# Kernel tuning notes

Measured on AMD Instinct MI355X. Metric: run time of the kernel, lower is better.

The kernel has to match this reference:

```python
import jax, jax.numpy as jnp
import numpy as np

N_LAYERS = 2
N_QUBITS = 4
BATCH = 1048576


def _apply1(state, U, w):
    # state: [B,2,2,2,2]; U: [2,2] (shared) or [B,2,2] (per-sample)
    s = jnp.moveaxis(state, w + 1, -1)
    if U.ndim == 3:
        s = jnp.einsum('bij,b...j->b...i', U, s)
    else:
        s = jnp.einsum('ij,...j->...i', U, s)
    return jnp.moveaxis(s, -1, w + 1)


_CNOT = np.array([[1, 0, 0, 0], [0, 1, 0, 0], [0, 0, 0, 1], [0, 0, 1, 0]], dtype=np.complex64)


def _cnot(state, c, t):
    s = jnp.moveaxis(state, (c + 1, t + 1), (-2, -1))
    sh = s.shape
    s = s.reshape(sh[:-2] + (4,))
    s = jnp.einsum('ij,...j->...i', jnp.asarray(_CNOT), s).reshape(sh)
    return jnp.moveaxis(s, (-2, -1), (c + 1, t + 1))


def _rx(theta):  # theta: [B] -> [B,2,2]
    c = jnp.cos(theta / 2).astype(jnp.complex64)
    s = (-1j * jnp.sin(theta / 2)).astype(jnp.complex64)
    return jnp.stack([jnp.stack([c, s], -1), jnp.stack([s, c], -1)], -2)


def _ry(theta):  # scalar -> [2,2]
    c = jnp.cos(theta / 2).astype(jnp.complex64)
    s = jnp.sin(theta / 2).astype(jnp.complex64)
    return jnp.stack([jnp.stack([c, -s]), jnp.stack([s, c])])


def _rz(theta):  # scalar -> [2,2] diagonal
    em = jnp.exp(-0.5j * theta.astype(jnp.complex64))
    ep = jnp.exp(0.5j * theta.astype(jnp.complex64))
    z = jnp.zeros((), jnp.complex64)
    return jnp.stack([jnp.stack([em, z]), jnp.stack([z, ep])])


def setup_inputs() -> dict:
    key = jax.random.key(0)
    k1, k2 = jax.random.split(key)
    x = jax.random.uniform(k1, (BATCH, N_QUBITS), jnp.float32) * (2.0 * np.pi)
    weights = jax.random.uniform(k2, (N_LAYERS, N_QUBITS, 2), jnp.float32) * (2.0 * np.pi)
    return {"x": x, "weights": weights}


def reference(x, weights):
    B = x.shape[0]
    # |0000> state, batched: [B,2,2,2,2]
    state = jnp.zeros((B, 16), jnp.complex64).at[:, 0].set(1.0)
    state = state.reshape((B,) + (2,) * N_QUBITS)
    for l in range(N_LAYERS):
        for i in range(N_QUBITS):
            state = _apply1(state, _rx(x[:, i]), i)
        for i in range(N_QUBITS):
            state = _apply1(state, _ry(weights[l, i, 0]), i)
            state = _apply1(state, _rz(weights[l, i, 1]), i)
        for i in range(N_QUBITS - 1):
            state = _cnot(state, i, i + 1)
    probs = state.real ** 2 + state.imag ** 2  # [B,2,2,2,2]
    outs = []
    for i in range(N_QUBITS):
        axes = tuple(a for a in range(1, N_QUBITS + 1) if a != i + 1)
        m = probs.sum(axes)  # [B,2]
        outs.append(m[:, 0] - m[:, 1])  # <Z_i>
    return jnp.stack(outs, -1)  # [B,4]
```

## Files before the change

kernel.cpp:

```cpp
#include <hip/hip_runtime.h>


struct C2 { float r, i; };

__device__ __forceinline__ C2 cmul(C2 a, C2 b) {
    C2 o;
    o.r = a.r * b.r - a.i * b.i;
    o.i = a.r * b.i + a.i * b.r;
    return o;
}

__global__ void precompute_gates(const float* __restrict__ w, float* __restrict__ g) {
    int t = threadIdx.x;
    if (t >= 8) return;
    int l = t >> 2, q = t & 3;
    float thy = w[l * 8 + q * 2 + 0];
    float thz = w[l * 8 + q * 2 + 1];
    float cy = cosf(0.5f * thy), sy = sinf(0.5f * thy);
    float cz = cosf(0.5f * thz), sz = sinf(0.5f * thz);
    float* o = g + l * 32 + q * 8;
    if (l == 0) {
        o[0] = cz * cy;  o[1] = -sz * cy;
        o[2] = sz * sy;  o[3] =  cz * sy;
        o[4] = cz * sy;  o[5] =  sz * sy;
        o[6] = sz * cy;  o[7] = -cz * cy;
    } else {
        o[0] =  cz * cy;  o[1] = -sz * cy;
        o[2] = -cz * sy;  o[3] =  sz * sy;
        o[4] =  cz * sy;  o[5] =  sz * sy;
        o[6] =  cz * cy;  o[7] =  sz * cy;
    }
}

__device__ __forceinline__ void cnot_chain(C2 st[16]) {
    #pragma unroll
    for (int j = 0; j < 4; j++) { C2 t = st[8 + j]; st[8 + j] = st[12 + j]; st[12 + j] = t; }
    {
        C2 t;
        t = st[4];  st[4]  = st[6];  st[6]  = t;
        t = st[5];  st[5]  = st[7];  st[7]  = t;
        t = st[12]; st[12] = st[14]; st[14] = t;
        t = st[13]; st[13] = st[15]; st[15] = t;
    }
    {
        C2 t;
        t = st[2];  st[2]  = st[3];  st[3]  = t;
        t = st[6];  st[6]  = st[7];  st[7]  = t;
        t = st[10]; st[10] = st[11]; st[11] = t;
        t = st[14]; st[14] = st[15]; st[15] = t;
    }
}

__global__ void __launch_bounds__(256) qml_kernel(
        const float* __restrict__ x, const float* __restrict__ g,
        float* __restrict__ out, int batch) {
    int tid = blockIdx.x * blockDim.x + threadIdx.x;
    if (tid >= batch) return;

    float4 xv = reinterpret_cast<const float4*>(x)[tid];
    float c[4], s[4];
    __sincosf(0.5f * xv.x, &s[0], &c[0]);
    __sincosf(0.5f * xv.y, &s[1], &c[1]);
    __sincosf(0.5f * xv.z, &s[2], &c[2]);
    __sincosf(0.5f * xv.w, &s[3], &c[3]);

    C2 v[4][2];
    #pragma unroll
    for (int q = 0; q < 4; q++) {
        const float* o = g + q * 8;
        v[q][0].r = c[q] * o[0] + s[q] * o[2];
        v[q][0].i = c[q] * o[1] + s[q] * o[3];
        v[q][1].r = c[q] * o[4] + s[q] * o[6];
        v[q][1].i = c[q] * o[5] + s[q] * o[7];
    }

    C2 t01[4], t23[4], st[16];
    #pragma unroll
    for (int a = 0; a < 2; a++)
        #pragma unroll
        for (int b = 0; b < 2; b++) {
            t01[a * 2 + b] = cmul(v[0][a], v[1][b]);
            t23[a * 2 + b] = cmul(v[2][a], v[3][b]);
        }
    #pragma unroll
    for (int a = 0; a < 4; a++)
        #pragma unroll
        for (int b = 0; b < 4; b++)
            st[a * 4 + b] = cmul(t01[a], t23[b]);

    cnot_chain(st);

    #pragma unroll
    for (int q = 0; q < 4; q++) {
        const float* o = g + 32 + q * 8;
        C2 u00, u01, u10, u11;
        u00.r = c[q] * o[0] + s[q] * o[3];
        u00.i = c[q] * o[1] - s[q] * o[2];
        u01.r = c[q] * o[2] + s[q] * o[1];
        u01.i = c[q] * o[3] - s[q] * o[0];
        u10.r = c[q] * o[4] + s[q] * o[7];
        u10.i = c[q] * o[5] - s[q] * o[6];
        u11.r = c[q] * o[6] + s[q] * o[5];
        u11.i = c[q] * o[7] - s[q] * o[4];
        int bit = 8 >> q;
        #pragma unroll
        for (int n0 = 0; n0 < 16; n0++) {
            if (n0 & bit) continue;
            int n1 = n0 | bit;
            C2 a0 = st[n0], a1 = st[n1];
            st[n0].r = u00.r * a0.r - u00.i * a0.i + u01.r * a1.r - u01.i * a1.i;
            st[n0].i = u00.r * a0.i + u00.i * a0.r + u01.r * a1.i + u01.i * a1.r;
            st[n1].r = u10.r * a0.r - u10.i * a0.i + u11.r * a1.r - u11.i * a1.i;
            st[n1].i = u10.r * a0.i + u10.i * a0.r + u11.r * a1.i + u11.i * a1.r;
        }
    }

    cnot_chain(st);

    float p[16];
    #pragma unroll
    for (int n = 0; n < 16; n++) p[n] = st[n].r * st[n].r + st[n].i * st[n].i;

    float a8[8], z3 = 0.f;
    #pragma unroll
    for (int m = 0; m < 8; m++) { a8[m] = p[2 * m] + p[2 * m + 1]; z3 += p[2 * m] - p[2 * m + 1]; }
    float b4[4], z2 = 0.f;
    #pragma unroll
    for (int k = 0; k < 4; k++) { b4[k] = a8[2 * k] + a8[2 * k + 1]; z2 += a8[2 * k] - a8[2 * k + 1]; }
    float z1 = (b4[0] - b4[1]) + (b4[2] - b4[3]);
    float z0 = (b4[0] + b4[1]) - (b4[2] + b4[3]);

    float4 ov = make_float4(z0, z1, z2, z3);
    reinterpret_cast<float4*>(out)[tid] = ov;
}

extern "C" void kernel_launch(void* const* d_in, const int* in_sizes, int n_in,
                              void* d_out, int out_size, void* d_ws, size_t ws_size,
                              hipStream_t stream) {
    const float* x = (const float*)d_in[0];
    const float* w = (const float*)d_in[1];
    float* out = (float*)d_out;
    float* g = (float*)d_ws;
    int batch = in_sizes[0] / 4;

    precompute_gates<<<1, 64, 0, stream>>>(w, g);
    int block = 256;
    int grid = (batch + block - 1) / block;
    qml_kernel<<<grid, block, 0, stream>>>(x, g, out, batch);
}
```

Baseline: 85.99 us.

## Process two samples per thread, simplify layer-2 gate algebra, use hardware sin/cos

Each thread now handles two batch samples, and the gate table is hoisted into registers once per thread. The second-layer gate (RZ·RY·RX) is reduced algebraically: the RZ phase is dropped because it does not affect Z-basis probabilities, so only cos/sin of the RY angle are stored. The per-sample sin/cos now use the raw AMDGCN sin/cos builtins on x/(4π), which removes the range-reduction code. The aim is to cut ALU work and global-load overhead per sample, at the cost of higher register pressure, half as many threads, and possible precision loss from the hardware transcendentals on larger arguments.

Result: slower. 92.54 us (+7.6%).

```diff
diff --git a/kernel.cpp b/kernel.cpp
--- a/kernel.cpp
+++ b/kernel.cpp
@@ -10,25 +10,26 @@
     return o;
 }
 
+#define INV_4PI 0.07957747154594767f
+
 __global__ void precompute_gates(const float* __restrict__ w, float* __restrict__ g) {
     int t = threadIdx.x;
     if (t >= 8) return;
     int l = t >> 2, q = t & 3;
-    float thy = w[l * 8 + q * 2 + 0];
-    float thz = w[l * 8 + q * 2 + 1];
-    float cy = cosf(0.5f * thy), sy = sinf(0.5f * thy);
-    float cz = cosf(0.5f * thz), sz = sinf(0.5f * thz);
-    float* o = g + l * 32 + q * 8;
     if (l == 0) {
+        float thy = w[q * 2 + 0];
+        float thz = w[q * 2 + 1];
+        float cy = cosf(0.5f * thy), sy = sinf(0.5f * thy);
+        float cz = cosf(0.5f * thz), sz = sinf(0.5f * thz);
+        float* o = g + q * 8;
         o[0] = cz * cy;  o[1] = -sz * cy;
         o[2] = sz * sy;  o[3] =  cz * sy;
         o[4] = cz * sy;  o[5] =  sz * sy;
         o[6] = sz * cy;  o[7] = -cz * cy;
     } else {
-        o[0] =  cz * cy;  o[1] = -sz * cy;
-        o[2] = -cz * sy;  o[3] =  sz * sy;
-        o[4] =  cz * sy;  o[5] =  sz * sy;
-        o[6] =  cz * cy;  o[7] =  sz * cy;
+        float thy = w[8 + q * 2 + 0];
+        g[32 + q * 2 + 0] = cosf(0.5f * thy);
+        g[32 + q * 2 + 1] = sinf(0.5f * thy);
     }
 }
 
@@ -54,84 +55,111 @@
 __global__ void __launch_bounds__(256) qml_kernel(
         const float* __restrict__ x, const float* __restrict__ g,
         float* __restrict__ out, int batch) {
-    int tid = blockIdx.x * blockDim.x + threadIdx.x;
-    if (tid >= batch) return;
+    int base = (blockIdx.x * blockDim.x + threadIdx.x) * 2;
+    if (base >= batch) return;
+    int idx1 = (base + 1 < batch) ? base + 1 : base;
 
-    float4 xv = reinterpret_cast<const float4*>(x)[tid];
-    float c[4], s[4];
-    __sincosf(0.5f * xv.x, &s[0], &c[0]);
-    __sincosf(0.5f * xv.y, &s[1], &c[1]);
-    __sincosf(0.5f * xv.z, &s[2], &c[2]);
-    __sincosf(0.5f * xv.w, &s[3], &c[3]);
+    float l1[32];
+    #pragma unroll
+    for (int j = 0; j < 32; j++) l1[j] = g[j];
+    float cb[4], sb[4];
+    #pragma unroll
+    for (int q = 0; q < 4; q++) { cb[q] = g[32 + q * 2]; sb[q] = g[33 + q * 2]; }
 
-    C2 v[4][2];
+    float4 xv[2];
+    xv[0] = reinterpret_cast<const float4*>(x)[base];
+    xv[1] = reinterpret_cast<const float4*>(x)[idx1];
+
+    float c[2][4], s[2][4];
     #pragma unroll
-    for (int q = 0; q < 4; q++) {
-        const float* o = g + q * 8;
-        v[q][0].r = c[q] * o[0] + s[q] * o[2];
-        v[q][0].i = c[q] * o[1] + s[q] * o[3];
-        v[q][1].r = c[q] * o[4] + s[q] * o[6];
-        v[q][1].i = c[q] * o[5] + s[q] * o[7];
+    for (int k = 0; k < 2; k++) {
+        float xs0 = xv[k].x, xs1 = xv[k].y, xs2 = xv[k].z, xs3 = xv[k].w;
+        float r0 = xs0 * INV_4PI, r1 = xs1 * INV_4PI, r2 = xs2 * INV_4PI, r3 = xs3 * INV_4PI;
+        s[k][0] = __builtin_amdgcn_sinf(r0); c[k][0] = __builtin_amdgcn_cosf(r0);
+        s[k][1] = __builtin_amdgcn_sinf(r1); c[k][1] = __builtin_amdgcn_cosf(r1);
+        s[k][2] = __builtin_amdgcn_sinf(r2); c[k][2] = __builtin_amdgcn_cosf(r2);
+        s[k][3] = __builtin_amdgcn_sinf(r3); c[k][3] = __builtin_amdgcn_cosf(r3);
     }
 
-    C2 t01[4], t23[4], st[16];
+    C2 v[2][4][2];
     #pragma unroll
-    for (int a = 0; a < 2; a++)
+    for (int k = 0; k < 2; k++)
         #pragma unroll
-        for (int b = 0; b < 2; b++) {
-            t01[a * 2 + b] = cmul(v[0][a], v[1][b]);
-            t23[a * 2 + b] = cmul(v[2][a], v[3][b]);
+        for (int q = 0; q < 4; q++) {
+            const float* o = l1 + q * 8;
+            v[k][q][0].r = c[k][q] * o[0] + s[k][q] * o[2];
+            v[k][q][0].i = c[k][q] * o[1] + s[k][q] * o[3];
+            v[k][q][1].r = c[k][q] * o[4] + s[k][q] * o[6];
+            v[k][q][1].i = c[k][q] * o[5] + s[k][q] * o[7];
         }
+
+    C2 st[2][16];
     #pragma unroll
-    for (int a = 0; a < 4; a++)
+    for (int k = 0; k < 2; k++) {
+        C2 t01[4], t23[4];
         #pragma unroll
-        for (int b = 0; b < 4; b++)
-            st[a * 4 + b] = cmul(t01[a], t23[b]);
+        for (int a = 0; a < 2; a++)
+            #pragma unroll
+            for (int b = 0; b < 2; b++) {
+                t01[a * 2 + b] = cmul(v[k][0][a], v[k][1][b]);
+                t23[a * 2 + b] = cmul(v[k][2][a], v[k][3][b]);
+            }
+        #pragma unroll
+        for (int a = 0; a < 4; a++)
+            #pragma unroll
+            for (int b = 0; b < 4; b++)
+                st[k][a * 4 + b] = cmul(t01[a], t23[b]);
+    }
 
-    cnot_chain(st);
+    #pragma unroll
+    for (int k = 0; k < 2; k++) cnot_chain(st[k]);
 
     #pragma unroll
     for (int q = 0; q < 4; q++) {
-        const float* o = g + 32 + q * 8;
-        C2 u00, u01, u10, u11;
-        u00.r = c[q] * o[0] + s[q] * o[3];
-        u00.i = c[q] * o[1] - s[q] * o[2];
-        u01.r = c[q] * o[2] + s[q] * o[1];
-        u01.i = c[q] * o[3] - s[q] * o[0];
-        u10.r = c[q] * o[4] + s[q] * o[7];
-        u10.i = c[q] * o[5] - s[q] * o[6];
-        u11.r = c[q] * o[6] + s[q] * o[5];
-        u11.i = c[q] * o[7] - s[q] * o[4];
         int bit = 8 >> q;
         #pragma unroll
-        for (int n0 = 0; n0 < 16; n0++) {
-            if (n0 & bit) continue;
-            int n1 = n0 | bit;
-            C2 a0 = st[n0], a1 = st[n1];
-            st[n0].r = u00.r * a0.r - u00.i * a0.i + u01.r * a1.r - u01.i * a1.i;
-            st[n0].i = u00.r * a0.i + u00.i * a0.r + u01.r * a1.i + u01.i * a1.r;
-            st[n1].r = u10.r * a0.r - u10.i * a0.i + u11.r * a1.r - u11.i * a1.i;
-            st[n1].i = u10.r * a0.i + u10.i * a0.r + u11.r * a1.i + u11.i * a1.r;
+        for (int k = 0; k < 2; k++) {
+            float ar =  cb[q] * c[k][q];
+            float ai =  sb[q] * s[k][q];
+            float br = -sb[q] * c[k][q];
+            float bi = -cb[q] * s[k][q];
+            #pragma unroll
+            for (int n0 = 0; n0 < 16; n0++) {
+                if (n0 & bit) continue;
+                int n1 = n0 | bit;
+                C2 a0 = st[k][n0], a1 = st[k][n1];
+                st[k][n0].r =  ar * a0.r - ai * a0.i + br * a1.r - bi * a1.i;
+                st[k][n0].i =  ar * a0.i + ai * a0.r + br * a1.i + bi * a1.r;
+                st[k][n1].r = -br * a0.r - bi * a0.i + ar * a1.r + ai * a1.i;
+                st[k][n1].i = -br * a0.i + bi * a0.r + ar * a1.i - ai * a1.r;
+            }
         }
     }
 
-    cnot_chain(st);
+    #pragma unroll
+    for (int k = 0; k < 2; k++) cnot_chain(st[k]);
 
-    float p[16];
+    float4 ov[2];
     #pragma unroll
-    for (int n = 0; n < 16; n++) p[n] = st[n].r * st[n].r + st[n].i * st[n].i;
+    for (int k = 0; k < 2; k++) {
+        float p[16];
+        #pragma unroll
+        for (int n = 0; n < 16; n++)
+            p[n] = st[k][n].r * st[k][n].r + st[k][n].i * st[k][n].i;
 
-    float a8[8], z3 = 0.f;
-    #pragma unroll
-    for (int m = 0; m < 8; m++) { a8[m] = p[2 * m] + p[2 * m + 1]; z3 += p[2 * m] - p[2 * m + 1]; }
-    float b4[4], z2 = 0.f;
-    #pragma unroll
-    for (int k = 0; k < 4; k++) { b4[k] = a8[2 * k] + a8[2 * k + 1]; z2 += a8[2 * k] - a8[2 * k + 1]; }
-    float z1 = (b4[0] - b4[1]) + (b4[2] - b4[3]);
-    float z0 = (b4[0] + b4[1]) - (b4[2] + b4[3]);
+        float a8[8], z3 = 0.f;
+        #pragma unroll
+        for (int m = 0; m < 8; m++) { a8[m] = p[2 * m] + p[2 * m + 1]; z3 += p[2 * m] - p[2 * m + 1]; }
+        float b4[4], z2 = 0.f;
+        #pragma unroll
+        for (int kk = 0; kk < 4; kk++) { b4[kk] = a8[2 * kk] + a8[2 * kk + 1]; z2 += a8[2 * kk] - a8[2 * kk + 1]; }
+        float z1 = (b4[0] - b4[1]) + (b4[2] - b4[3]);
+        float z0 = (b4[0] + b4[1]) - (b4[2] + b4[3]);
+        ov[k] = make_float4(z0, z1, z2, z3);
+    }
 
-    float4 ov = make_float4(z0, z1, z2, z3);
-    reinterpret_cast<float4*>(out)[tid] = ov;
+    reinterpret_cast<float4*>(out)[base] = ov[0];
+    reinterpret_cast<float4*>(out)[idx1] = ov[1];
 }
 
 extern "C" void kernel_launch(void* const* d_in, const int* in_sizes, int n_in,
@@ -145,6 +173,7 @@
 
     precompute_gates<<<1, 64, 0, stream>>>(w, g);
     int block = 256;
-    int grid = (batch + block - 1) / block;
+    int threads_needed = (batch + 1) / 2;
+    int grid = (threads_needed + block - 1) / block;
     qml_kernel<<<grid, block, 0, stream>>>(x, g, out, batch);
 }
```

## Eliminate layer-2 RZ phases and final qubit gate algebraically in readout

Applied to the files above, without the earlier changes.

Layer-2 RZ rotations are dropped for qubits 0-2 because diagonal phases before the final CNOTs and Z measurement do not change the expectation values. The last qubit's RX·RY·RZ gate is folded into closed-form coefficients applied to pairwise densities, and the second CNOT chain is absorbed into the reduction signs. Sines and cosines now use the raw hardware sin/cos builtins with a revolution-scaled argument instead of __sincosf. This cuts ALU work per sample in what is likely a memory-bound kernel, at the cost of a derivation that is hard to verify and depends on the hardware trig accuracy.

Result: slower. 94.20 us (+9.5%).

```diff
diff --git a/kernel.cpp b/kernel.cpp
--- a/kernel.cpp
+++ b/kernel.cpp
@@ -10,25 +10,31 @@
     return o;
 }
 
+#define INV_4PI 0.07957747154594767f
+
 __global__ void precompute_gates(const float* __restrict__ w, float* __restrict__ g) {
     int t = threadIdx.x;
     if (t >= 8) return;
     int l = t >> 2, q = t & 3;
-    float thy = w[l * 8 + q * 2 + 0];
-    float thz = w[l * 8 + q * 2 + 1];
-    float cy = cosf(0.5f * thy), sy = sinf(0.5f * thy);
-    float cz = cosf(0.5f * thz), sz = sinf(0.5f * thz);
-    float* o = g + l * 32 + q * 8;
     if (l == 0) {
+        float thy = w[q * 2 + 0];
+        float thz = w[q * 2 + 1];
+        float cy = cosf(0.5f * thy), sy = sinf(0.5f * thy);
+        float cz = cosf(0.5f * thz), sz = sinf(0.5f * thz);
+        float* o = g + q * 8;
         o[0] = cz * cy;  o[1] = -sz * cy;
         o[2] = sz * sy;  o[3] =  cz * sy;
         o[4] = cz * sy;  o[5] =  sz * sy;
         o[6] = sz * cy;  o[7] = -cz * cy;
+    } else if (q < 3) {
+        float thy = w[8 + q * 2 + 0];
+        g[32 + q * 2 + 0] = cosf(0.5f * thy);
+        g[32 + q * 2 + 1] = sinf(0.5f * thy);
     } else {
-        o[0] =  cz * cy;  o[1] = -sz * cy;
-        o[2] = -cz * sy;  o[3] =  sz * sy;
-        o[4] =  cz * sy;  o[5] =  sz * sy;
-        o[6] =  cz * cy;  o[7] =  sz * cy;
+        float thy = w[8 + 3 * 2 + 0];
+        g[40] =  cosf(thy);
+        g[41] = -2.0f * sinf(thy);
+        g[42] =  4.0f * cosf(thy);
     }
 }
 
@@ -59,10 +65,14 @@
 
     float4 xv = reinterpret_cast<const float4*>(x)[tid];
     float c[4], s[4];
-    __sincosf(0.5f * xv.x, &s[0], &c[0]);
-    __sincosf(0.5f * xv.y, &s[1], &c[1]);
-    __sincosf(0.5f * xv.z, &s[2], &c[2]);
-    __sincosf(0.5f * xv.w, &s[3], &c[3]);
+    {
+        float r0 = xv.x * INV_4PI, r1 = xv.y * INV_4PI;
+        float r2 = xv.z * INV_4PI, r3 = xv.w * INV_4PI;
+        s[0] = __builtin_amdgcn_sinf(r0); c[0] = __builtin_amdgcn_cosf(r0);
+        s[1] = __builtin_amdgcn_sinf(r1); c[1] = __builtin_amdgcn_cosf(r1);
+        s[2] = __builtin_amdgcn_sinf(r2); c[2] = __builtin_amdgcn_cosf(r2);
+        s[3] = __builtin_amdgcn_sinf(r3); c[3] = __builtin_amdgcn_cosf(r3);
+    }
 
     C2 v[4][2];
     #pragma unroll
@@ -91,47 +101,59 @@
     cnot_chain(st);
 
     #pragma unroll
-    for (int q = 0; q < 4; q++) {
-        const float* o = g + 32 + q * 8;
-        C2 u00, u01, u10, u11;
-        u00.r = c[q] * o[0] + s[q] * o[3];
-        u00.i = c[q] * o[1] - s[q] * o[2];
-        u01.r = c[q] * o[2] + s[q] * o[1];
-        u01.i = c[q] * o[3] - s[q] * o[0];
-        u10.r = c[q] * o[4] + s[q] * o[7];
-        u10.i = c[q] * o[5] - s[q] * o[6];
-        u11.r = c[q] * o[6] + s[q] * o[5];
-        u11.i = c[q] * o[7] - s[q] * o[4];
+    for (int q = 0; q < 3; q++) {
+        float cb = g[32 + q * 2 + 0];
+        float sb = g[32 + q * 2 + 1];
+        float ar =  cb * c[q];
+        float ai =  sb * s[q];
+        float br = -sb * c[q];
+        float bi = -cb * s[q];
         int bit = 8 >> q;
         #pragma unroll
         for (int n0 = 0; n0 < 16; n0++) {
             if (n0 & bit) continue;
             int n1 = n0 | bit;
             C2 a0 = st[n0], a1 = st[n1];
-            st[n0].r = u00.r * a0.r - u00.i * a0.i + u01.r * a1.r - u01.i * a1.i;
-            st[n0].i = u00.r * a0.i + u00.i * a0.r + u01.r * a1.i + u01.i * a1.r;
-            st[n1].r = u10.r * a0.r - u10.i * a0.i + u11.r * a1.r - u11.i * a1.i;
-            st[n1].i = u10.r * a0.i + u10.i * a0.r + u11.r * a1.i + u11.i * a1.r;
+            st[n0].r =  ar * a0.r - ai * a0.i + br * a1.r - bi * a1.i;
+            st[n0].i =  ar * a0.i + ai * a0.r + br * a1.i + bi * a1.r;
+            st[n1].r = -br * a0.r - bi * a0.i + ar * a1.r + ai * a1.i;
+            st[n1].i = -br * a0.i + bi * a0.r + ar * a1.i - ai * a1.r;
         }
     }
 
-    cnot_chain(st);
+    float m_coef, cu, cv;
+    {
+        float cs2 = __builtin_fmaf(-s[3], s[3], c[3] * c[3]);
+        m_coef = g[40] * cs2;
+        cu = g[41];
+        cv = g[42] * (c[3] * s[3]);
+    }
 
-    float p[16];
+    float S[8], D[8];
     #pragma unroll
-    for (int n = 0; n < 16; n++) p[n] = st[n].r * st[n].r + st[n].i * st[n].i;
+    for (int m = 0; m < 8; m++) {
+        C2 a0 = st[2 * m], a1 = st[2 * m + 1];
+        float q0 = __builtin_fmaf(a0.i, a0.i, a0.r * a0.r);
+        float q1 = __builtin_fmaf(a1.i, a1.i, a1.r * a1.r);
+        float Rc = __builtin_fmaf(a0.i, a1.i, a0.r * a1.r);
+        float Ic = __builtin_fmaf(-a0.i, a1.r, a0.r * a1.i);
+        S[m] = q0 + q1;
+        float dd = q0 - q1;
+        float Dm = m_coef * dd;
+        Dm = __builtin_fmaf(cu, Rc, Dm);
+        Dm = __builtin_fmaf(cv, Ic, Dm);
+        D[m] = Dm;
+    }
 
-    float a8[8], z3 = 0.f;
-    #pragma unroll
-    for (int m = 0; m < 8; m++) { a8[m] = p[2 * m] + p[2 * m + 1]; z3 += p[2 * m] - p[2 * m + 1]; }
-    float b4[4], z2 = 0.f;
-    #pragma unroll
-    for (int k = 0; k < 4; k++) { b4[k] = a8[2 * k] + a8[2 * k + 1]; z2 += a8[2 * k] - a8[2 * k + 1]; }
-    float z1 = (b4[0] - b4[1]) + (b4[2] - b4[3]);
-    float z0 = (b4[0] + b4[1]) - (b4[2] + b4[3]);
+    float e0 = S[0] + S[1], e1 = S[2] + S[3], e2 = S[4] + S[5], e3 = S[6] + S[7];
+    float z0 = (e0 + e1) - (e2 + e3);
+    float z1 = (e0 - e1) - (e2 - e3);
+    float f0 = S[0] - S[1], f1 = S[2] - S[3], f2 = S[4] - S[5], f3 = S[6] - S[7];
+    float z2 = (f0 - f1) - (f2 - f3);
+    float g0 = D[0] - D[1], g1 = D[2] - D[3], g2 = D[4] - D[5], g3 = D[6] - D[7];
+    float z3 = (g0 - g1) - (g2 - g3);
 
-    float4 ov = make_float4(z0, z1, z2, z3);
-    reinterpret_cast<float4*>(out)[tid] = ov;
+    reinterpret_cast<float4*>(out)[tid] = make_float4(z0, z1, z2, z3);
 }
 
 extern "C" void kernel_launch(void* const* d_in, const int* in_sizes, int n_in,
```

## Use packed float2 math and simplify layer-2 gate to RY·RX product form

Applied to the files above, without the earlier changes.

Represents complex amplitudes as 2-wide float vectors so multiplies map to packed FMA instructions (v_pk_fma_f32 on CDNA). The second layer's RZ is dropped from the per-sample gate because diagonal phases before measurement do not affect probabilities. The combined RY·RX matrix is expressed with four real coefficients instead of eight precomputed values. This reduces per-thread ALU work and constant loads, at the risk of extra shuffle/negate instructions if the compiler does not fuse swizzles into packed ops. The kernel is likely memory-bound, so the gain may be small.

Result: slower. 88.25 us (+2.6%).

```diff
diff --git a/kernel.cpp b/kernel.cpp
--- a/kernel.cpp
+++ b/kernel.cpp
@@ -1,49 +1,54 @@
 #include <hip/hip_runtime.h>
 
 
-struct C2 { float r, i; };
+typedef float v2f __attribute__((ext_vector_type(2)));
 
-__device__ __forceinline__ C2 cmul(C2 a, C2 b) {
-    C2 o;
-    o.r = a.r * b.r - a.i * b.i;
-    o.i = a.r * b.i + a.i * b.r;
-    return o;
+__device__ __forceinline__ v2f splat2(float a) { v2f r; r.x = a; r.y = a; return r; }
+
+__device__ __forceinline__ v2f pfma(float a, v2f b, v2f c) {
+    return __builtin_elementwise_fma(splat2(a), b, c);
+}
+
+__device__ __forceinline__ v2f swneg(v2f a) { return __builtin_shufflevector(a, -a, 3, 0); }
+__device__ __forceinline__ v2f swconj(v2f a) { return __builtin_shufflevector(a, -a, 1, 2); }
+
+__device__ __forceinline__ v2f cmul(v2f a, v2f b) {
+    return pfma(a.x, b, splat2(a.y) * swneg(b));
 }
 
 __global__ void precompute_gates(const float* __restrict__ w, float* __restrict__ g) {
     int t = threadIdx.x;
     if (t >= 8) return;
     int l = t >> 2, q = t & 3;
-    float thy = w[l * 8 + q * 2 + 0];
-    float thz = w[l * 8 + q * 2 + 1];
-    float cy = cosf(0.5f * thy), sy = sinf(0.5f * thy);
-    float cz = cosf(0.5f * thz), sz = sinf(0.5f * thz);
-    float* o = g + l * 32 + q * 8;
     if (l == 0) {
+        float thy = w[q * 2 + 0];
+        float thz = w[q * 2 + 1];
+        float cy = cosf(0.5f * thy), sy = sinf(0.5f * thy);
+        float cz = cosf(0.5f * thz), sz = sinf(0.5f * thz);
+        float* o = g + q * 8;
         o[0] = cz * cy;  o[1] = -sz * cy;
         o[2] = sz * sy;  o[3] =  cz * sy;
         o[4] = cz * sy;  o[5] =  sz * sy;
         o[6] = sz * cy;  o[7] = -cz * cy;
     } else {
-        o[0] =  cz * cy;  o[1] = -sz * cy;
-        o[2] = -cz * sy;  o[3] =  sz * sy;
-        o[4] =  cz * sy;  o[5] =  sz * sy;
-        o[6] =  cz * cy;  o[7] =  sz * cy;
+        float thy = w[8 + q * 2 + 0];
+        g[32 + q * 2 + 0] = cosf(0.5f * thy);
+        g[32 + q * 2 + 1] = sinf(0.5f * thy);
     }
 }
 
-__device__ __forceinline__ void cnot_chain(C2 st[16]) {
+__device__ __forceinline__ void cnot_chain(v2f st[16]) {
     #pragma unroll
-    for (int j = 0; j < 4; j++) { C2 t = st[8 + j]; st[8 + j] = st[12 + j]; st[12 + j] = t; }
+    for (int j = 0; j < 4; j++) { v2f t = st[8 + j]; st[8 + j] = st[12 + j]; st[12 + j] = t; }
     {
-        C2 t;
+        v2f t;
         t = st[4];  st[4]  = st[6];  st[6]  = t;
         t = st[5];  st[5]  = st[7];  st[7]  = t;
         t = st[12]; st[12] = st[14]; st[14] = t;
         t = st[13]; st[13] = st[15]; st[15] = t;
     }
     {
-        C2 t;
+        v2f t;
         t = st[2];  st[2]  = st[3];  st[3]  = t;
         t = st[6];  st[6]  = st[7];  st[7]  = t;
         t = st[10]; st[10] = st[11]; st[11] = t;
@@ -64,17 +69,15 @@
     __sincosf(0.5f * xv.z, &s[2], &c[2]);
     __sincosf(0.5f * xv.w, &s[3], &c[3]);
 
-    C2 v[4][2];
+    const v2f* __restrict__ gv = reinterpret_cast<const v2f*>(g);
+    v2f v[4][2];
     #pragma unroll
     for (int q = 0; q < 4; q++) {
-        const float* o = g + q * 8;
-        v[q][0].r = c[q] * o[0] + s[q] * o[2];
-        v[q][0].i = c[q] * o[1] + s[q] * o[3];
-        v[q][1].r = c[q] * o[4] + s[q] * o[6];
-        v[q][1].i = c[q] * o[5] + s[q] * o[7];
+        v[q][0] = pfma(c[q], gv[q * 4 + 0], splat2(s[q]) * gv[q * 4 + 1]);
+        v[q][1] = pfma(c[q], gv[q * 4 + 2], splat2(s[q]) * gv[q * 4 + 3]);
     }
 
-    C2 t01[4], t23[4], st[16];
+    v2f t01[4], t23[4], st[16];
     #pragma unroll
     for (int a = 0; a < 2; a++)
         #pragma unroll
@@ -92,26 +95,23 @@
 
     #pragma unroll
     for (int q = 0; q < 4; q++) {
-        const float* o = g + 32 + q * 8;
-        C2 u00, u01, u10, u11;
-        u00.r = c[q] * o[0] + s[q] * o[3];
-        u00.i = c[q] * o[1] - s[q] * o[2];
-        u01.r = c[q] * o[2] + s[q] * o[1];
-        u01.i = c[q] * o[3] - s[q] * o[0];
-        u10.r = c[q] * o[4] + s[q] * o[7];
-        u10.i = c[q] * o[5] - s[q] * o[6];
-        u11.r = c[q] * o[6] + s[q] * o[5];
-        u11.i = c[q] * o[7] - s[q] * o[4];
+        float cb = g[32 + q * 2 + 0];
+        float sb = g[32 + q * 2 + 1];
+        float ar  = cb * c[q];
+        float ai  = sb * s[q];
+        float nbr = sb * c[q];
+        float nbi = cb * s[q];
+        float br = -nbr, bi = -nbi;
         int bit = 8 >> q;
         #pragma unroll
         for (int n0 = 0; n0 < 16; n0++) {
             if (n0 & bit) continue;
             int n1 = n0 | bit;
-            C2 a0 = st[n0], a1 = st[n1];
-            st[n0].r = u00.r * a0.r - u00.i * a0.i + u01.r * a1.r - u01.i * a1.i;
-            st[n0].i = u00.r * a0.i + u00.i * a0.r + u01.r * a1.i + u01.i * a1.r;
-            st[n1].r = u10.r * a0.r - u10.i * a0.i + u11.r * a1.r - u11.i * a1.i;
-            st[n1].i = u10.r * a0.i + u10.i * a0.r + u11.r * a1.i + u11.i * a1.r;
+            v2f a0 = st[n0], a1 = st[n1];
+            v2f a0n = swneg(a0),  a1n = swneg(a1);
+            v2f a0c = swconj(a0), a1c = swconj(a1);
+            st[n0] = pfma(ar,  a0, pfma(ai,  a0n, pfma(br, a1, splat2(bi) * a1n)));
+            st[n1] = pfma(nbr, a0, pfma(nbi, a0c, pfma(ar, a1, splat2(ai) * a1c)));
         }
     }
 
@@ -119,7 +119,10 @@
 
     float p[16];
     #pragma unroll
-    for (int n = 0; n < 16; n++) p[n] = st[n].r * st[n].r + st[n].i * st[n].i;
+    for (int n = 0; n < 16; n++) {
+        v2f sq = st[n] * st[n];
+        p[n] = sq.x + sq.y;
+    }
 
     float a8[8], z3 = 0.f;
     #pragma unroll
@@ -130,8 +133,7 @@
     float z1 = (b4[0] - b4[1]) + (b4[2] - b4[3]);
     float z0 = (b4[0] + b4[1]) - (b4[2] + b4[3]);
 
-    float4 ov = make_float4(z0, z1, z2, z3);
-    reinterpret_cast<float4*>(out)[tid] = ov;
+    reinterpret_cast<float4*>(out)[tid] = make_float4(z0, z1, z2, z3);
 }
 
 extern "C" void kernel_launch(void* const* d_in, const int* in_sizes, int n_in,
```
